# Kernel optimization log

Hardware: AMD Instinct MI355X
Metric: run time of the kernel (lower is better)

## Reference

```python
import jax, jax.numpy as jnp
import numpy as np
import math

B, S, D, H, L, DFF, NHEADS_OUT = 2, 1024, 1024, 16, 4, 4096, 3
DK = D // H
LN_EPS = 1e-5


def setup_inputs() -> dict:
    key = jax.random.key(0)
    ks = jax.random.split(key, 16)
    w = lambda k, shp: jax.random.normal(k, shp, dtype=jnp.float32) * 0.02
    return {
        "src": jax.random.normal(ks[0], (B, S, 1), dtype=jnp.float32),
        "emb_w": w(ks[1], (1, D)), "emb_b": jnp.zeros((D,), jnp.float32),
        "pe": w(ks[2], (S, D)),
        "Wq": w(ks[3], (L, D, D)), "bq": jnp.zeros((L, D), jnp.float32),
        "Wk": w(ks[4], (L, D, D)), "bk": jnp.zeros((L, D), jnp.float32),
        "Wv": w(ks[5], (L, D, D)), "bv": jnp.zeros((L, D), jnp.float32),
        "Wo": w(ks[6], (L, D, D)), "bo": jnp.zeros((L, D), jnp.float32),
        "fc1_w": w(ks[7], (L, D, DFF)), "fc1_b": jnp.zeros((L, DFF), jnp.float32),
        "fc2_w": w(ks[8], (L, DFF, D)), "fc2_b": jnp.zeros((L, D), jnp.float32),
        "ln1_g": jnp.ones((L, D), jnp.float32), "ln1_b": jnp.zeros((L, D), jnp.float32),
        "ln2_g": jnp.ones((L, D), jnp.float32), "ln2_b": jnp.zeros((L, D), jnp.float32),
        "hw1": w(ks[9], (NHEADS_OUT, D, D)), "hb1": jnp.zeros((NHEADS_OUT, D), jnp.float32),
        "hw2": w(ks[10], (NHEADS_OUT, D, 1)), "hb2": jnp.zeros((NHEADS_OUT, 1), jnp.float32),
    }


def _layernorm(x, g, b):
    mu = jnp.mean(x, axis=-1, keepdims=True)
    var = jnp.mean((x - mu) ** 2, axis=-1, keepdims=True)
    return (x - mu) * jax.lax.rsqrt(var + LN_EPS) * g + b


def _custom_softmax(x):
    # faithful to module's custom_softmax: max (inf->0), exp, sum + 1e-9
    m = jnp.max(x, axis=-1, keepdims=True)
    m = jnp.where(jnp.isinf(m), 0.0, m)
    e = jnp.exp(x - m)
    return e / (jnp.sum(e, axis=-1, keepdims=True) + 1e-9)


def _attention(x, Wq, bq, Wk, bk, Wv, bv, Wo, bo, mask):
    b, s, d = x.shape
    split = lambda t: t.reshape(b, s, H, DK).transpose(0, 2, 1, 3)  # [B,H,S,DK]
    q = split(x @ Wq + bq)
    k = split(x @ Wk + bk)
    v = split(x @ Wv + bv)
    scores = jnp.einsum('bhqd,bhkd->bhqk', q, k) / math.sqrt(DK)
    scores = jnp.where(mask, scores, -jnp.inf)
    probs = _custom_softmax(scores)
    out = jnp.einsum('bhqk,bhkd->bhqd', probs, v)
    out = out.transpose(0, 2, 1, 3).reshape(b, s, d)
    return out @ Wo + bo


def reference(src, emb_w, emb_b, pe, Wq, bq, Wk, bk, Wv, bv, Wo, bo,
              fc1_w, fc1_b, fc2_w, fc2_b, ln1_g, ln1_b, ln2_g, ln2_b,
              hw1, hb1, hw2, hb2):
    s = src.shape[1]
    mask = jnp.tril(jnp.ones((s, s), dtype=bool))[None, None]  # causal [1,1,S,S]
    x = src @ emb_w + emb_b          # [B,S,D]
    x = x + pe[:s]                   # learned positional encoding
    for l in range(L):
        attn = _attention(x, Wq[l], bq[l], Wk[l], bk[l], Wv[l], bv[l], Wo[l], bo[l], mask)
        h = _layernorm(x + attn, ln1_g[l], ln1_b[l])
        x = h + attn                 # quirk in original forward_step
        ff = jax.nn.relu(jax.nn.relu(x @ fc1_w[l] + fc1_b[l]) @ fc2_w[l] + fc2_b[l])
        h2 = _layernorm(x + ff, ln2_g[l], ln2_b[l])
        x = h2 + ff                  # quirk in original forward_step
    # output_size independent 2-layer heads, each -> scalar; stack on last dim
    hid = jax.nn.relu(jnp.einsum('bsd,odf->bsof', x, hw1) + hb1[None, None])  # [B,S,3,D]
    out = jnp.einsum('bsof,ofe->bsoe', hid, hw2) + hb2[None, None]            # [B,S,3,1]
    return out[..., 0]               # [B,S,3]
```

## Files before the change

### kernel.cpp

```cpp
#include <hip/hip_runtime.h>
#include <hip/hip_bf16.h>


#define BB 2
#define SS 1024
#define DD 1024
#define HH 16
#define LL 4
#define DFFC 4096
#define DKC 64

typedef __attribute__((ext_vector_type(8))) short short8;
typedef __attribute__((ext_vector_type(4))) float f32x4;

#define GLD16(gptr, ldsptr) \
    __builtin_amdgcn_global_load_lds( \
        (const __attribute__((address_space(1))) unsigned int*)(gptr), \
        (__attribute__((address_space(3))) unsigned int*)(ldsptr), 16, 0, 0)

__device__ __forceinline__ float ldin(const void* p, long long i, int isbf) {
    if (isbf) {
        unsigned int u = ((unsigned int)((const unsigned short*)p)[i]) << 16;
        return __uint_as_float(u);
    }
    return ((const float*)p)[i];
}
__device__ __forceinline__ unsigned short f2bf(float f) {
    unsigned int u = __float_as_uint(f);
    return (unsigned short)((u + 0x7FFFu + ((u >> 16) & 1u)) >> 16);
}
__device__ __forceinline__ float bf2f(unsigned short h) {
    return __uint_as_float(((unsigned int)h) << 16);
}

__global__ void k_detect(const void* __restrict__ ln1g, int* __restrict__ flag) {
    unsigned int w = *(const unsigned int*)ln1g;
    *flag = (w == 0x3F800000u) ? 0 : 1;
}

__global__ void k_embed(const void* __restrict__ src, const void* __restrict__ emb_w,
                        const void* __restrict__ emb_b, const void* __restrict__ pe,
                        float* __restrict__ x, unsigned short* __restrict__ xb,
                        const int* __restrict__ flag) {
    int row = blockIdx.x;
    int s = row & (SS - 1);
    int isbf = *flag;
    float sv = ldin(src, row, isbf);
    for (int d = threadIdx.x; d < DD; d += 256) {
        float v = sv * ldin(emb_w, d, isbf) + ldin(emb_b, d, isbf) + ldin(pe, (long long)s * DD + d, isbf);
        x[(long long)row * DD + d] = v;
        xb[(long long)row * DD + d] = f2bf(v);
    }
}

struct TSlot { const void* src; long long off; int ldw; int nrows; int ncols; long long dstoff; };
struct TArgs { TSlot s[4]; };

__global__ __launch_bounds__(256) void k_wtrans(TArgs ta, unsigned short* __restrict__ dst,
                                                const int* __restrict__ flag) {
    TSlot sl = ta.s[blockIdx.z];
    if (!sl.src) return;
    int k0 = blockIdx.x * 64, n0 = blockIdx.y * 64;
    if (k0 >= sl.nrows || n0 >= sl.ncols) return;
    int isbf = *flag;
    __shared__ float tile[64][65];
    int tid = threadIdx.x;
    int c = tid & 63, rg = tid >> 6;
    #pragma unroll
    for (int i = 0; i < 16; i++) {
        int kr = rg * 16 + i;
        tile[kr][c] = ldin(sl.src, sl.off + (long long)(k0 + kr) * sl.ldw + n0 + c, isbf);
    }
    __syncthreads();
    int nr = tid >> 2, kc = (tid & 3) * 16;
    unsigned short* dp = dst + sl.dstoff + (long long)(n0 + nr) * sl.nrows + k0 + kc;
    unsigned short h[16];
    #pragma unroll
    for (int j = 0; j < 16; j++) h[j] = f2bf(tile[kc + j][nr]);
    uint4 u0, u1;
    u0.x = h[0] | (h[1] << 16);  u0.y = h[2] | (h[3] << 16);
    u0.z = h[4] | (h[5] << 16);  u0.w = h[6] | (h[7] << 16);
    u1.x = h[8] | (h[9] << 16);  u1.y = h[10] | (h[11] << 16);
    u1.z = h[12] | (h[13] << 16); u1.w = h[14] | (h[15] << 16);
    *(uint4*)&dp[0] = u0;
    *(uint4*)&dp[8] = u1;
}

template <int MF, int NF>
__global__ __launch_bounds__(256) void k_gemm_mfma(
    const unsigned short* __restrict__ A, int lda,
    const unsigned short* __restrict__ Wt,
    const void* b0, const void* b1, const void* b2,
    long long o0, long long o1, long long o2,
    float* __restrict__ C, int ldc,
    unsigned short* __restrict__ Cb, int ldcb,
    int K, int act, int accum, const int* __restrict__ flag)
{
    const int BM = 32 * MF;
    const int BN = 32 * NF;
    __shared__ __align__(16) unsigned short As[2][BM * 32];
    __shared__ __align__(16) unsigned short Bs[2][BN * 32];
    int bflag = *flag;
    int tid = threadIdx.x;
    int wave = tid >> 6, lane = tid & 63, quad = lane >> 4, l16 = lane & 15;
    int wm = (wave & 1) * 16 * MF, wn = (wave >> 1) * 16 * NF;
    int bm = blockIdx.y * BM, bn = blockIdx.x * BN;
    int srow = lane >> 2;
    int scol = (lane & 3) * 8;

    f32x4 acc[MF][NF];
    #pragma unroll
    for (int i = 0; i < MF; i++)
        #pragma unroll
        for (int j = 0; j < NF; j++) acc[i][j] = (f32x4){0.f, 0.f, 0.f, 0.f};

    const unsigned short* Abase = A + (size_t)bm * lda;

    auto stage = [&](int k0, int p) {
        #pragma unroll
        for (int i = 0; i < MF / 2; i++) {
            int s = wave * (MF / 2) + i;
            GLD16(Abase + (size_t)(s * 16 + srow) * lda + k0 + scol, &As[p][(s * 16) * 32]);
        }
        #pragma unroll
        for (int i = 0; i < NF / 2; i++) {
            int s = wave * (NF / 2) + i;
            GLD16(Wt + (size_t)(bn + s * 16 + srow) * K + k0 + scol, &Bs[p][(s * 16) * 32]);
        }
    };

    int nk = K >> 5;
    stage(0, 0);
    for (int it = 0; it < nk; it++) {
        int p = it & 1;
        __syncthreads();
        if (it + 1 < nk) stage((it + 1) << 5, p ^ 1);

        short8 af[MF], bf[NF];
        #pragma unroll
        for (int mi = 0; mi < MF; mi++)
            af[mi] = *(const short8*)&As[p][(wm + mi * 16 + l16) * 32 + quad * 8];
        #pragma unroll
        for (int ni = 0; ni < NF; ni++)
            bf[ni] = *(const short8*)&Bs[p][(wn + ni * 16 + l16) * 32 + quad * 8];
        #pragma unroll
        for (int mi = 0; mi < MF; mi++)
            #pragma unroll
            for (int ni = 0; ni < NF; ni++)
                acc[mi][ni] = __builtin_amdgcn_mfma_f32_16x16x32_bf16(af[mi], bf[ni], acc[mi][ni], 0, 0, 0);
    }

    #pragma unroll
    for (int ni = 0; ni < NF; ni++) {
        int cn = bn + wn + ni * 16 + l16;
        float bval = 0.0f;
        if (b0) {
            int sel = cn >> 10;
            const void* bp = (sel == 0) ? b0 : (sel == 1) ? b1 : b2;
            long long oo = (sel == 0) ? o0 : (sel == 1) ? o1 : o2;
            bval = ldin(bp, oo + (cn - (sel << 10)), bflag);
        }
        #pragma unroll
        for (int mi = 0; mi < MF; mi++) {
            #pragma unroll
            for (int rr = 0; rr < 4; rr++) {
                int cm = bm + wm + mi * 16 + quad * 4 + rr;
                float v = acc[mi][ni][rr] + bval;
                if (accum) v += C[(size_t)cm * ldc + cn];
                if (act) v = fmaxf(v, 0.0f);
                if (C) C[(size_t)cm * ldc + cn] = v;
                if (Cb) Cb[(size_t)cm * ldcb + cn] = f2bf(v);
            }
        }
    }
}

__global__ __launch_bounds__(256) void k_attn(const unsigned short* __restrict__ qkv,
                                              float* __restrict__ part0,
                                              float* __restrict__ part1,
                                              float* __restrict__ rs)
{
    __shared__ __align__(16) unsigned short Vt[2][64 * 72];
    __shared__ __align__(16) unsigned short Ps[4][16 * 72];

    int tid = threadIdx.x;
    int wave = tid >> 6, lane = tid & 63, quad = lane >> 4, l16 = lane & 15;

    int flat = blockIdx.x + (blockIdx.y << 4) + (blockIdx.z << 9);
    int xcd = flat & 7;
    int j = flat >> 3;
    int bh = ((j >> 5) << 3) + xcd;
    int r = j & 31;
    int split = r >> 4;
    int qt = 15 - (r & 15);

    int b = bh >> 4, h = bh & 15;
    int q0 = qt * 64;
    int qbase = q0 + wave * 16;

    int nk = qt + 1;
    int half = (nk + 1) >> 1;
    int kt0 = split ? half : 0;
    int kt1 = split ? nk : half;

    const unsigned short* qrow = qkv + (size_t)(b * SS + qbase + l16) * 3072 + h * DKC;
    short8 aq0 = *(const short8*)(qrow + quad * 8);
    short8 aq1 = *(const short8*)(qrow + 32 + quad * 8);

    f32x4 oacc[4];
    #pragma unroll
    for (int nt = 0; nt < 4; nt++) oacc[nt] = (f32x4){0.f, 0.f, 0.f, 0.f};
    float rsum[4] = {0.f, 0.f, 0.f, 0.f};

    int kp = tid & 31;
    int vc = (tid >> 5) * 8;
    unsigned short* pw = &Ps[wave][0];

    short8 vs0, vs1;
    auto loadV = [&](int k0) {
        const unsigned short* v0 = qkv + (size_t)(b * SS + k0 + 2 * kp) * 3072 + 2048 + h * DKC + vc;
        vs0 = *(const short8*)v0;
        vs1 = *(const short8*)(v0 + 3072);
    };
    auto writeV = [&](int p) {
        unsigned int* vt32 = (unsigned int*)&Vt[p][0];
        #pragma unroll
        for (int i = 0; i < 8; i++) {
            unsigned int pr = ((unsigned int)(unsigned short)vs0[i]) |
                              (((unsigned int)(unsigned short)vs1[i]) << 16);
            vt32[(vc + i) * 36 + kp] = pr;
        }
    };

    short8 kc0[4], kc1[4];
    auto loadK = [&](int k0, short8 (&d0)[4], short8 (&d1)[4]) {
        #pragma unroll
        for (int nt = 0; nt < 4; nt++) {
            const unsigned short* krow =
                qkv + (size_t)(b * SS + k0 + nt * 16 + l16) * 3072 + 1024 + h * DKC + quad * 8;
            d0[nt] = *(const short8*)(krow);
            d1[nt] = *(const short8*)(krow + 32);
        }
    };

    if (kt0 < kt1) {
        loadV(kt0 * 64);
        loadK(kt0 * 64, kc0, kc1);
        writeV(0);
    }
    for (int kt = kt0; kt < kt1; kt++) {
        int k0 = kt * 64;
        int p = (kt - kt0) & 1;
        __syncthreads();

        short8 kn0[4], kn1[4];
        int havenext = (kt + 1 < kt1);
        if (havenext) {
            loadV(k0 + 64);
            loadK(k0 + 64, kn0, kn1);
        }

        f32x4 sacc[4];
        #pragma unroll
        for (int nt = 0; nt < 4; nt++) {
            sacc[nt] = (f32x4){0.f, 0.f, 0.f, 0.f};
            sacc[nt] = __builtin_amdgcn_mfma_f32_16x16x32_bf16(aq0, kc0[nt], sacc[nt], 0, 0, 0);
            sacc[nt] = __builtin_amdgcn_mfma_f32_16x16x32_bf16(aq1, kc1[nt], sacc[nt], 0, 0, 0);
        }

        #pragma unroll
        for (int nt = 0; nt < 4; nt++) {
            int key = k0 + nt * 16 + l16;
            #pragma unroll
            for (int rr = 0; rr < 4; rr++) {
                float pv = __expf(sacc[nt][rr] * 0.125f);
                if (key > qbase + quad * 4 + rr) pv = 0.0f;
                rsum[rr] += pv;
                pw[(quad * 4 + rr) * 72 + nt * 16 + l16] = f2bf(pv);
            }
        }

        short8 ap0 = *(const short8*)&pw[l16 * 72 + quad * 8];
        short8 ap1 = *(const short8*)&pw[l16 * 72 + 32 + quad * 8];
        #pragma unroll
        for (int nt = 0; nt < 4; nt++) {
            short8 bv0 = *(const short8*)&Vt[p][(nt * 16 + l16) * 72 + quad * 8];
            short8 bv1 = *(const short8*)&Vt[p][(nt * 16 + l16) * 72 + 32 + quad * 8];
            oacc[nt] = __builtin_amdgcn_mfma_f32_16x16x32_bf16(ap0, bv0, oacc[nt], 0, 0, 0);
            oacc[nt] = __builtin_amdgcn_mfma_f32_16x16x32_bf16(ap1, bv1, oacc[nt], 0, 0, 0);
        }

        if (havenext) {
            writeV(p ^ 1);
            #pragma unroll
            for (int nt = 0; nt < 4; nt++) { kc0[nt] = kn0[nt]; kc1[nt] = kn1[nt]; }
        }
    }

    #pragma unroll
    for (int m = 1; m < 16; m <<= 1) {
        #pragma unroll
        for (int rr = 0; rr < 4; rr++)
            rsum[rr] += __shfl_xor(rsum[rr], m, 64);
    }
    float* part = split ? part1 : part0;
    #pragma unroll
    for (int rr = 0; rr < 4; rr++) {
        int q = qbase + quad * 4 + rr;
        size_t obase = (size_t)(b * SS + q) * 1024 + h * DKC;
        #pragma unroll
        for (int nt = 0; nt < 4; nt++)
            part[obase + nt * 16 + l16] = oacc[nt][rr];
        if (l16 == 0)
            rs[(((size_t)split * 2 + b) * 16 + h) * 1024 + q] = rsum[rr];
    }
}

__global__ __launch_bounds__(256) void k_comb(const float* __restrict__ p0,
                                              const float* __restrict__ p1,
                                              const float* __restrict__ rs,
                                              unsigned short* __restrict__ qkv)
{
    int row = blockIdx.x;
    int b = row >> 10, q = row & 1023;
    int tid = threadIdx.x;
    int col = tid * 4;
    int h = col >> 6;
    float r0 = rs[(((size_t)0 + b) * 16 + h) * 1024 + q];
    float r1 = rs[(((size_t)2 + b) * 16 + h) * 1024 + q];
    float inv = 1.0f / (r0 + r1 + 1e-9f);
    size_t base = (size_t)row * 1024 + col;
    float4 a = *(const float4*)(p0 + base);
    float4 c = *(const float4*)(p1 + base);
    unsigned short* dst = qkv + (size_t)row * 3072 + col;
    uint2 w;
    w.x = f2bf((a.x + c.x) * inv) | (f2bf((a.y + c.y) * inv) << 16);
    w.y = f2bf((a.z + c.z) * inv) | (f2bf((a.w + c.w) * inv) << 16);
    *(uint2*)dst = w;
}

__global__ __launch_bounds__(256) void k_addlnadd(float* __restrict__ x, const float* __restrict__ t,
                                                  const void* __restrict__ g, long long goff,
                                                  const void* __restrict__ bta, long long boff,
                                                  unsigned short* __restrict__ xb,
                                                  const int* __restrict__ flag)
{
    int row = blockIdx.x;
    int tid = threadIdx.x;
    int isbf = *flag;
    __shared__ float red[256];
    long long base = (long long)row * DD;

    float yv[4], tv[4];
    float lsum = 0.0f;
    #pragma unroll
    for (int i = 0; i < 4; i++) {
        int d = tid + i * 256;
        tv[i] = t[base + d];
        yv[i] = x[base + d] + tv[i];
        lsum += yv[i];
    }
    red[tid] = lsum;
    __syncthreads();
    for (int s = 128; s > 0; s >>= 1) {
        if (tid < s) red[tid] += red[tid + s];
        __syncthreads();
    }
    float mu = red[0] * (1.0f / DD);
    __syncthreads();

    float lv = 0.0f;
    #pragma unroll
    for (int i = 0; i < 4; i++) {
        float dl = yv[i] - mu;
        lv += dl * dl;
    }
    red[tid] = lv;
    __syncthreads();
    for (int s = 128; s > 0; s >>= 1) {
        if (tid < s) red[tid] += red[tid + s];
        __syncthreads();
    }
    float rs = rsqrtf(red[0] * (1.0f / DD) + 1e-5f);

    #pragma unroll
    for (int i = 0; i < 4; i++) {
        int d = tid + i * 256;
        float nrm = (yv[i] - mu) * rs * ldin(g, goff + d, isbf) + ldin(bta, boff + d, isbf);
        float xo = nrm + tv[i];
        x[base + d] = xo;
        xb[base + d] = f2bf(xo);
    }
}

__global__ __launch_bounds__(256) void k_head(const unsigned short* __restrict__ hid,
                                              const void* __restrict__ hw2,
                                              const void* __restrict__ hb2,
                                              void* __restrict__ out,
                                              const int* __restrict__ flag)
{
    int row = blockIdx.x;
    int o = blockIdx.y;
    int tid = threadIdx.x;
    int isbf = *flag;
    __shared__ float red[256];
    long long base = (long long)row * 3072 + o * 1024;
    float acc = 0.0f;
    for (int f = tid; f < DD; f += 256)
        acc += bf2f(hid[base + f]) * ldin(hw2, (long long)o * DD + f, isbf);
    red[tid] = acc;
    __syncthreads();
    for (int s = 128; s > 0; s >>= 1) {
        if (tid < s) red[tid] += red[tid + s];
        __syncthreads();
    }
    if (tid == 0) {
        float r = red[0] + ldin(hb2, o, isbf);
        long long idx = (long long)row * 3 + o;
        if (isbf) ((__hip_bfloat16*)out)[idx] = __float2bfloat16(r);
        else      ((float*)out)[idx] = r;
    }
}

extern "C" void kernel_launch(void* const* d_in, const int* in_sizes, int n_in,
                              void* d_out, int out_size, void* d_ws, size_t ws_size,
                              hipStream_t stream) {
    char* w = (char*)d_ws;
    int* flag = (int*)w;
    const size_t NA = (size_t)BB * SS * DD;
    float* x  = (float*)(w + 256);
    float* tb = x + NA;
    unsigned short* qkv = (unsigned short*)(tb + NA);
    unsigned short* hb  = qkv + (size_t)BB * SS * 3072;
    unsigned short* wbuf = hb + (size_t)BB * SS * 2048;
    unsigned short* xb = wbuf + 4 * (size_t)DD * DD;
    float* rsbuf = (float*)(xb + NA);

    const long long MM = (long long)DD * DD;
    dim3 blk(256);
    TSlot z = {nullptr, 0, 1, 0, 0, 0};

    k_detect<<<1, 1, 0, stream>>>(d_in[16], flag);
    k_embed<<<BB * SS, blk, 0, stream>>>(d_in[0], d_in[1], d_in[2], d_in[3], x, xb, flag);

    for (int l = 0; l < LL; l++) {
        long long wo = (long long)l * MM;
        long long bo = (long long)l * DD;
        {
            TArgs ta = {{ {d_in[4],  wo, DD, DD, DD, 0},
                          {d_in[6],  wo, DD, DD, DD, MM},
                          {d_in[8],  wo, DD, DD, DD, 2 * MM},
                          {d_in[10], wo, DD, DD, DD, 3 * MM} }};
            k_wtrans<<<dim3(16, 16, 4), blk, 0, stream>>>(ta, wbuf, flag);
        }
        k_gemm_mfma<4, 2><<<dim3(48, 16), blk, 0, stream>>>(
            xb, DD, wbuf, d_in[5], d_in[7], d_in[9], bo, bo, bo,
            nullptr, 0, qkv, 3072, DD, 0, 0, flag);
        k_attn<<<dim3(16, BB * HH, 2), blk, 0, stream>>>(qkv, tb, (float*)hb, rsbuf);
        k_comb<<<BB * SS, blk, 0, stream>>>(tb, (float*)hb, rsbuf, qkv);
        k_gemm_mfma<2, 2><<<dim3(16, 32), blk, 0, stream>>>(
            qkv, 3072, wbuf + 3 * MM, d_in[11], d_in[11], d_in[11], bo, bo, bo,
            tb, DD, nullptr, 0, DD, 0, 0, flag);
        k_addlnadd<<<BB * SS, blk, 0, stream>>>(x, tb, d_in[16], bo, d_in[17], bo, xb, flag);
        for (int c = 0; c < 2; c++) {
            long long w1off = (long long)l * DD * DFFC + (long long)c * 2048;
            long long b1off = (long long)l * DFFC + (long long)c * 2048;
            long long w2off = (long long)l * DFFC * DD + (long long)c * 2048 * DD;
            {
                TArgs ta = {{ {d_in[12], w1off, DFFC, DD, 2048, 0},
                              {d_in[14], w2off, DD, 2048, DD, 2 * MM}, z, z }};
                k_wtrans<<<dim3(32, 32, 2), blk, 0, stream>>>(ta, wbuf, flag);
            }
            k_gemm_mfma<4, 2><<<dim3(32, 16), blk, 0, stream>>>(
                xb, DD, wbuf, d_in[13], d_in[13], d_in[13], b1off, b1off + 1024, 0,
                nullptr, 0, hb, 2048, DD, 1, 0, flag);
            k_gemm_mfma<2, 2><<<dim3(16, 32), blk, 0, stream>>>(
                hb, 2048, wbuf + 2 * MM,
                (c == 1) ? d_in[15] : nullptr, d_in[15], d_in[15], bo, bo, bo,
                tb, DD, nullptr, 0, 2048, (c == 1) ? 1 : 0, c, flag);
        }
        k_addlnadd<<<BB * SS, blk, 0, stream>>>(x, tb, d_in[18], bo, d_in[19], bo, xb, flag);
    }

    {
        TArgs ta = {{ {d_in[20], 0 * MM, DD, DD, DD, 0},
                      {d_in[20], 1 * MM, DD, DD, DD, MM},
                      {d_in[20], 2 * MM, DD, DD, DD, 2 * MM}, z }};
        k_wtrans<<<dim3(16, 16, 3), blk, 0, stream>>>(ta, wbuf, flag);
    }
    k_gemm_mfma<4, 2><<<dim3(48, 16), blk, 0, stream>>>(
        xb, DD, wbuf, d_in[21], d_in[21], d_in[21], 0, 1024, 2048,
        nullptr, 0, qkv, 3072, DD, 1, 0, flag);
    k_head<<<dim3(BB * SS, 3), blk, 0, stream>>>(qkv, d_in[22], d_in[23], d_out, flag);
}
```

Before: 1.200 ms.

## Split-K atomic GEMMs, larger tiles, full-width FFN and bias/relu folded into LayerNorm

Widens the GEMM tiles to 128x128 (4x4 MFMA fragments per wave). The out-projection and fc2 GEMMs now use split-K across blockIdx.z, accumulating into a buffer zeroed beforehand with float atomics. The fc2 bias and ReLU move into the add-LayerNorm kernel. The FFN is no longer chunked in two: fc1 output for the full DFF width goes into the qkv buffer, and each weight matrix is transposed once per layer. This cuts kernel launches and the read-modify-write accumulate pass, and raises work per block. It adds atomic traffic, a zeroing pass, a non-deterministic summation order, and higher register pressure from the larger tile.

```diff
diff --git a/kernel.cpp b/kernel.cpp
--- a/kernel.cpp
+++ b/kernel.cpp
@@ -32,10 +32,17 @@
 __device__ __forceinline__ float bf2f(unsigned short h) {
     return __uint_as_float(((unsigned int)h) << 16);
 }
+__device__ __forceinline__ void atomAddF(float* p, float v) {
+    __hip_atomic_fetch_add(p, v, __ATOMIC_RELAXED, __HIP_MEMORY_SCOPE_AGENT);
+}
 
 __global__ void k_detect(const void* __restrict__ ln1g, int* __restrict__ flag) {
     unsigned int w = *(const unsigned int*)ln1g;
     *flag = (w == 0x3F800000u) ? 0 : 1;
+}
+
+__global__ __launch_bounds__(256) void k_zero(float4* __restrict__ p) {
+    p[(size_t)blockIdx.x * 256 + threadIdx.x] = make_float4(0.f, 0.f, 0.f, 0.f);
 }
 
 __global__ void k_embed(const void* __restrict__ src, const void* __restrict__ emb_w,
@@ -86,15 +93,16 @@
     *(uint4*)&dp[8] = u1;
 }
 
+struct BiasArgs { const void* p[4]; long long o[4]; };
+
 template <int MF, int NF>
 __global__ __launch_bounds__(256) void k_gemm_mfma(
     const unsigned short* __restrict__ A, int lda,
-    const unsigned short* __restrict__ Wt,
-    const void* b0, const void* b1, const void* b2,
-    long long o0, long long o1, long long o2,
-    float* __restrict__ C, int ldc,
+    const unsigned short* __restrict__ Wt, int ktot,
+    int ksplit, BiasArgs ba,
+    float* __restrict__ C, int ldc, int atomicC,
     unsigned short* __restrict__ Cb, int ldcb,
-    int K, int act, int accum, const int* __restrict__ flag)
+    int act, const int* __restrict__ flag)
 {
     const int BM = 32 * MF;
     const int BN = 32 * NF;
@@ -105,6 +113,7 @@
     int wave = tid >> 6, lane = tid & 63, quad = lane >> 4, l16 = lane & 15;
     int wm = (wave & 1) * 16 * MF, wn = (wave >> 1) * 16 * NF;
     int bm = blockIdx.y * BM, bn = blockIdx.x * BN;
+    int kb = blockIdx.z * ksplit;
     int srow = lane >> 2;
     int scol = (lane & 3) * 8;
 
@@ -114,7 +123,7 @@
         #pragma unroll
         for (int j = 0; j < NF; j++) acc[i][j] = (f32x4){0.f, 0.f, 0.f, 0.f};
 
-    const unsigned short* Abase = A + (size_t)bm * lda;
+    const unsigned short* Abase = A + (size_t)bm * lda + kb;
 
     auto stage = [&](int k0, int p) {
         #pragma unroll
@@ -125,11 +134,11 @@
         #pragma unroll
         for (int i = 0; i < NF / 2; i++) {
             int s = wave * (NF / 2) + i;
-            GLD16(Wt + (size_t)(bn + s * 16 + srow) * K + k0 + scol, &Bs[p][(s * 16) * 32]);
+            GLD16(Wt + (size_t)(bn + s * 16 + srow) * ktot + kb + k0 + scol, &Bs[p][(s * 16) * 32]);
         }
     };
 
-    int nk = K >> 5;
+    int nk = ksplit >> 5;
     stage(0, 0);
     for (int it = 0; it < nk; it++) {
         int p = it & 1;
@@ -154,11 +163,9 @@
     for (int ni = 0; ni < NF; ni++) {
         int cn = bn + wn + ni * 16 + l16;
         float bval = 0.0f;
-        if (b0) {
+        if (ba.p[0]) {
             int sel = cn >> 10;
-            const void* bp = (sel == 0) ? b0 : (sel == 1) ? b1 : b2;
-            long long oo = (sel == 0) ? o0 : (sel == 1) ? o1 : o2;
-            bval = ldin(bp, oo + (cn - (sel << 10)), bflag);
+            bval = ldin(ba.p[sel], ba.o[sel] + (cn & 1023), bflag);
         }
         #pragma unroll
         for (int mi = 0; mi < MF; mi++) {
@@ -166,10 +173,13 @@
             for (int rr = 0; rr < 4; rr++) {
                 int cm = bm + wm + mi * 16 + quad * 4 + rr;
                 float v = acc[mi][ni][rr] + bval;
-                if (accum) v += C[(size_t)cm * ldc + cn];
                 if (act) v = fmaxf(v, 0.0f);
-                if (C) C[(size_t)cm * ldc + cn] = v;
-                if (Cb) Cb[(size_t)cm * ldcb + cn] = f2bf(v);
+                if (atomicC) {
+                    atomAddF(&C[(size_t)cm * ldc + cn], v);
+                } else {
+                    if (C) C[(size_t)cm * ldc + cn] = v;
+                    if (Cb) Cb[(size_t)cm * ldcb + cn] = f2bf(v);
+                }
             }
         }
     }
@@ -340,6 +350,7 @@
 }
 
 __global__ __launch_bounds__(256) void k_addlnadd(float* __restrict__ x, const float* __restrict__ t,
+                                                  const void* __restrict__ tbias, long long tboff, int tact,
                                                   const void* __restrict__ g, long long goff,
                                                   const void* __restrict__ bta, long long boff,
                                                   unsigned short* __restrict__ xb,
@@ -356,8 +367,10 @@
     #pragma unroll
     for (int i = 0; i < 4; i++) {
         int d = tid + i * 256;
-        tv[i] = t[base + d];
-        yv[i] = x[base + d] + tv[i];
+        float tt = t[base + d] + ldin(tbias, tboff + d, isbf);
+        if (tact) tt = fmaxf(tt, 0.0f);
+        tv[i] = tt;
+        yv[i] = x[base + d] + tt;
         lsum += yv[i];
     }
     red[tid] = lsum;
@@ -381,12 +394,12 @@
         if (tid < s) red[tid] += red[tid + s];
         __syncthreads();
     }
-    float rs = rsqrtf(red[0] * (1.0f / DD) + 1e-5f);
+    float rsq = rsqrtf(red[0] * (1.0f / DD) + 1e-5f);
 
     #pragma unroll
     for (int i = 0; i < 4; i++) {
         int d = tid + i * 256;
-        float nrm = (yv[i] - mu) * rs * ldin(g, goff + d, isbf) + ldin(bta, boff + d, isbf);
+        float nrm = (yv[i] - mu) * rsq * ldin(g, goff + d, isbf) + ldin(bta, boff + d, isbf);
         float xo = nrm + tv[i];
         x[base + d] = xo;
         xb[base + d] = f2bf(xo);
@@ -435,10 +448,12 @@
     unsigned short* wbuf = hb + (size_t)BB * SS * 2048;
     unsigned short* xb = wbuf + 4 * (size_t)DD * DD;
     float* rsbuf = (float*)(xb + NA);
+    unsigned short* f1 = qkv;
 
     const long long MM = (long long)DD * DD;
     dim3 blk(256);
     TSlot z = {nullptr, 0, 1, 0, 0, 0};
+    BiasArgs nb = {{nullptr, nullptr, nullptr, nullptr}, {0, 0, 0, 0}};
 
     k_detect<<<1, 1, 0, stream>>>(d_in[16], flag);
     k_embed<<<BB * SS, blk, 0, stream>>>(d_in[0], d_in[1], d_in[2], d_in[3], x, xb, flag);
@@ -453,33 +468,38 @@
                           {d_in[10], wo, DD, DD, DD, 3 * MM} }};
             k_wtrans<<<dim3(16, 16, 4), blk, 0, stream>>>(ta, wbuf, flag);
         }
-        k_gemm_mfma<4, 2><<<dim3(48, 16), blk, 0, stream>>>(
-            xb, DD, wbuf, d_in[5], d_in[7], d_in[9], bo, bo, bo,
-            nullptr, 0, qkv, 3072, DD, 0, 0, flag);
+        {
+            BiasArgs qb = {{d_in[5], d_in[7], d_in[9], nullptr}, {bo, bo, bo, 0}};
+            k_gemm_mfma<4, 4><<<dim3(24, 16), blk, 0, stream>>>(
+                xb, DD, wbuf, DD, DD, qb, nullptr, 0, 0, qkv, 3072, 0, flag);
+        }
         k_attn<<<dim3(16, BB * HH, 2), blk, 0, stream>>>(qkv, tb, (float*)hb, rsbuf);
         k_comb<<<BB * SS, blk, 0, stream>>>(tb, (float*)hb, rsbuf, qkv);
-        k_gemm_mfma<2, 2><<<dim3(16, 32), blk, 0, stream>>>(
-            qkv, 3072, wbuf + 3 * MM, d_in[11], d_in[11], d_in[11], bo, bo, bo,
-            tb, DD, nullptr, 0, DD, 0, 0, flag);
-        k_addlnadd<<<BB * SS, blk, 0, stream>>>(x, tb, d_in[16], bo, d_in[17], bo, xb, flag);
-        for (int c = 0; c < 2; c++) {
-            long long w1off = (long long)l * DD * DFFC + (long long)c * 2048;
-            long long b1off = (long long)l * DFFC + (long long)c * 2048;
-            long long w2off = (long long)l * DFFC * DD + (long long)c * 2048 * DD;
-            {
-                TArgs ta = {{ {d_in[12], w1off, DFFC, DD, 2048, 0},
-                              {d_in[14], w2off, DD, 2048, DD, 2 * MM}, z, z }};
-                k_wtrans<<<dim3(32, 32, 2), blk, 0, stream>>>(ta, wbuf, flag);
-            }
-            k_gemm_mfma<4, 2><<<dim3(32, 16), blk, 0, stream>>>(
-                xb, DD, wbuf, d_in[13], d_in[13], d_in[13], b1off, b1off + 1024, 0,
-                nullptr, 0, hb, 2048, DD, 1, 0, flag);
-            k_gemm_mfma<2, 2><<<dim3(16, 32), blk, 0, stream>>>(
-                hb, 2048, wbuf + 2 * MM,
-                (c == 1) ? d_in[15] : nullptr, d_in[15], d_in[15], bo, bo, bo,
-                tb, DD, nullptr, 0, 2048, (c == 1) ? 1 : 0, c, flag);
-        }
-        k_addlnadd<<<BB * SS, blk, 0, stream>>>(x, tb, d_in[18], bo, d_in[19], bo, xb, flag);
+        k_zero<<<2048, blk, 0, stream>>>((float4*)tb);
+        k_gemm_mfma<4, 4><<<dim3(8, 16, 4), blk, 0, stream>>>(
+            qkv, 3072, wbuf + 3 * MM, DD, 256, nb, tb, DD, 1, nullptr, 0, 0, flag);
+        k_addlnadd<<<BB * SS, blk, 0, stream>>>(x, tb, d_in[11], bo, 0,
+                                                d_in[16], bo, d_in[17], bo, xb, flag);
+        {
+            TArgs ta = {{ {d_in[12], (long long)l * DD * DFFC, DFFC, DD, DFFC, 0}, z, z, z }};
+            k_wtrans<<<dim3(16, 64, 1), blk, 0, stream>>>(ta, wbuf, flag);
+        }
+        {
+            long long f1b0 = (long long)l * DFFC;
+            BiasArgs fb = {{d_in[13], d_in[13], d_in[13], d_in[13]},
+                           {f1b0, f1b0 + 1024, f1b0 + 2048, f1b0 + 3072}};
+            k_gemm_mfma<4, 4><<<dim3(32, 16), blk, 0, stream>>>(
+                xb, DD, wbuf, DD, DD, fb, nullptr, 0, 0, f1, DFFC, 1, flag);
+        }
+        {
+            TArgs ta = {{ {d_in[14], (long long)l * DFFC * DD, DD, DFFC, DD, 0}, z, z, z }};
+            k_wtrans<<<dim3(64, 16, 1), blk, 0, stream>>>(ta, wbuf, flag);
+        }
+        k_zero<<<2048, blk, 0, stream>>>((float4*)tb);
+        k_gemm_mfma<4, 4><<<dim3(8, 16, 4), blk, 0, stream>>>(
+            f1, DFFC, wbuf, DFFC, 1024, nb, tb, DD, 1, nullptr, 0, 0, flag);
+        k_addlnadd<<<BB * SS, blk, 0, stream>>>(x, tb, d_in[15], bo, 1,
+                                                d_in[18], bo, d_in[19], bo, xb, flag);
     }
 
     {
@@ -488,8 +508,10 @@
                       {d_in[20], 2 * MM, DD, DD, DD, 2 * MM}, z }};
         k_wtrans<<<dim3(16, 16, 3), blk, 0, stream>>>(ta, wbuf, flag);
     }
-    k_gemm_mfma<4, 2><<<dim3(48, 16), blk, 0, stream>>>(
-        xb, DD, wbuf, d_in[21], d_in[21], d_in[21], 0, 1024, 2048,
-        nullptr, 0, qkv, 3072, DD, 1, 0, flag);
+    {
+        BiasArgs hbias = {{d_in[21], d_in[21], d_in[21], nullptr}, {0, 1024, 2048, 0}};
+        k_gemm_mfma<4, 4><<<dim3(24, 16), blk, 0, stream>>>(
+            xb, DD, wbuf, DD, DD, hbias, nullptr, 0, 0, qkv, 3072, 1, flag);
+    }
     k_head<<<dim3(BB * SS, 3), blk, 0, stream>>>(qkv, d_in[22], d_in[23], d_out, flag);
 }
```

New measurement: 1.225 ms. 1.02x slower.
